# Kernel optimization log

Measured on AMD Instinct MI355X. Metric: run time of the kernel, lower is better.

The kernel has to match this reference:

```python
import jax, jax.numpy as jnp
import numpy as np
from jax import lax

GN_EPS = 1e-5


def _conv2d(x, w, b, pad):
    # x: (N, C, H, W), w: (O, I, kh, kw)
    y = lax.conv_general_dilated(x, w, window_strides=(1, 1),
                                 padding=[(pad, pad), (pad, pad)],
                                 dimension_numbers=('NCHW', 'OIHW', 'NCHW'))
    return y + b[None, :, None, None]


def _eca(x, eca_w, eca_b):
    # x: (N, C, H, W) -> channel attention (N, C, 1, 1)
    y = jnp.mean(x, axis=(2, 3))[:, None, :]  # (N, 1, C) : GAP then treat C as length
    y = lax.conv_general_dilated(y, eca_w, window_strides=(1,),
                                 padding=[(1, 1)],
                                 dimension_numbers=('NCH', 'OIH', 'NCH'))
    y = jax.nn.sigmoid(y + eca_b[None, :, None])  # (N, 1, C)
    return y[:, 0, :, None, None]  # (N, C, 1, 1)


def _group_norm_per_channel(x, gn_w, gn_b):
    # num_groups == num_channels: normalize each channel over (H, W)
    mean = jnp.mean(x, axis=(2, 3), keepdims=True)
    var = jnp.var(x, axis=(2, 3), keepdims=True)
    xhat = (x - mean) * lax.rsqrt(var + GN_EPS)
    return xhat * gn_w[None, :, None, None] + gn_b[None, :, None, None]


def setup_inputs() -> dict:
    key = jax.random.key(0)
    ks = jax.random.split(key, 8)
    b, c, h, w = 16, 512, 64, 64
    cg = c // 32  # 16
    s = 1.0 / np.sqrt(cg)
    return {
        'x': jax.random.normal(ks[0], (b, c, h, w), jnp.float32),
        'conv1x1_w': jax.random.normal(ks[1], (cg, cg, 1, 1), jnp.float32) * s,
        'conv1x1_b': jnp.zeros((cg,), jnp.float32),
        'conv3x3_w': jax.random.normal(ks[2], (cg, cg, 3, 3), jnp.float32) * (s / 3),
        'conv3x3_b': jnp.zeros((cg,), jnp.float32),
        'conv5x5_w': jax.random.normal(ks[3], (cg, cg, 5, 5), jnp.float32) * (s / 5),
        'conv5x5_b': jnp.zeros((cg,), jnp.float32),
        'gn_w': jnp.ones((cg,), jnp.float32),
        'gn_b': jnp.zeros((cg,), jnp.float32),
        'eca_w': jax.random.normal(ks[4], (1, 1, 3), jnp.float32) * 0.5,
        'eca_b': jnp.zeros((1,), jnp.float32),
        'groups': 32,
    }


def reference(x, conv1x1_w, conv1x1_b, conv3x3_w, conv3x3_b,
              conv5x5_w, conv5x5_b, gn_w, gn_b, eca_w, eca_b, groups):
    b, c, h, w = x.shape
    cg = c // groups
    bg = b * groups
    group_x = x.reshape(bg, cg, h, w)

    # coordinate attention branch
    x_h = jnp.mean(group_x, axis=3, keepdims=True)            # (bg, cg, h, 1)
    x_w = jnp.mean(group_x, axis=2, keepdims=True)            # (bg, cg, 1, w)
    x_w_t = jnp.transpose(x_w, (0, 1, 3, 2))                  # (bg, cg, w, 1)
    hw = _conv2d(jnp.concatenate([x_h, x_w_t], axis=2), conv1x1_w, conv1x1_b, 0)
    x_h2, x_w2 = hw[:, :, :h, :], hw[:, :, h:, :]             # (bg,cg,h,1), (bg,cg,w,1)
    gated = group_x * jax.nn.sigmoid(x_h2) * jax.nn.sigmoid(jnp.transpose(x_w2, (0, 1, 3, 2)))
    x1 = _group_norm_per_channel(gated, gn_w, gn_b)

    # parallel conv branches
    x2 = _conv2d(group_x, conv3x3_w, conv3x3_b, 1)
    x3 = _conv2d(group_x, conv5x5_w, conv5x5_b, 2)

    # shared ECA channel attention over the three branches
    ca = _eca(x1, eca_w, eca_b) + _eca(x2, eca_w, eca_b) + _eca(x3, eca_w, eca_b)
    group_x = group_x * ca

    # cross-scale softmax-bmm interactions
    def chan_softmax(v):
        # (bg, cg, h, w) -> softmax over channel means -> (bg, 1, cg)
        return jax.nn.softmax(jnp.mean(v, axis=(2, 3)), axis=-1)[:, None, :]

    x11, x21, x31 = chan_softmax(x1), chan_softmax(x2), chan_softmax(x3)
    f1 = x1.reshape(bg, cg, h * w)
    f2 = x2.reshape(bg, cg, h * w)
    f3 = x3.reshape(bg, cg, h * w)

    weights = (jnp.matmul(x11, f2) + jnp.matmul(x11, f3)
               + jnp.matmul(x21, f1) + jnp.matmul(x21, f3)
               + jnp.matmul(x31, f1) + jnp.matmul(x31, f2))  # (bg, 1, h*w)
    weights = jax.nn.sigmoid(weights.reshape(bg, 1, h, w))

    return (group_x * weights).reshape(b, c, h, w)
```

## Files before the change

kernel.cpp:

```cpp
#include <hip/hip_runtime.h>

typedef unsigned int u32;

#define CG  16
#define HWN 4096

__device__ __forceinline__ float sigm(float x) { return 1.0f / (1.0f + __expf(-x)); }

union SharedU {
  struct { float row[16][64]; float col[16][64]; float cpart[16][8][64]; } p0;
  struct { float row[16][64]; float col[16][64]; float RS[16][25]; float part2[16][16]; float part3[16][16]; } p1;
  float band[8][20][72];
};

__global__ __launch_bounds__(256, 2) void ema_kernel(
    const float* __restrict__ x,
    const float* __restrict__ w1, const float* __restrict__ b1,
    const float* __restrict__ w3, const float* __restrict__ b3,
    const float* __restrict__ w5, const float* __restrict__ b5,
    const float* __restrict__ gnw, const float* __restrict__ gnb,
    const float* __restrict__ ew, const float* __restrict__ eb,
    float* __restrict__ out)
{
  __shared__ SharedU U;
  __shared__ float s_sh[16][64];
  __shared__ float s_sw[16][64];
  __shared__ float s_W5[16][28];
  __shared__ float s_ca[16], s_A1[16], s_Cc[16];
  __shared__ float s_w1[256], s_b1[16], s_gnw[16], s_gnb[16], s_b3[16], s_b5[16], s_ecaw[3], s_ecab[1];
  __shared__ float s_m2[16], s_m3[16], s_sm1[16], s_sm2[16], s_sm3[16];
  __shared__ float s_a1[16], s_a2[16], s_a3[16], s_total[16];
  __shared__ float s_red[16][4][2];
  __shared__ float s_scal[2];

  const int g = blockIdx.x;
  const int t = threadIdx.x;
  const float* px   = x   + (size_t)g * CG * HWN;
  float*       pout = out + (size_t)g * CG * HWN;

  {
    const int j = t & 31, half = t >> 5;
    for (int c = 0; c < CG; ++c) {
      float ca0 = 0.f, ca1 = 0.f;
      for (int k = 0; k < 8; ++k) {
        const int y = half * 8 + k;
        float2 v = *(const float2*)(px + c * HWN + y * 64 + 2 * j);
        ca0 += v.x; ca1 += v.y;
        float rp = v.x + v.y;
        rp += __shfl_xor(rp, 1);  rp += __shfl_xor(rp, 2);
        rp += __shfl_xor(rp, 4);  rp += __shfl_xor(rp, 8);
        rp += __shfl_xor(rp, 16);
        if (j == 0) U.p0.row[c][y] = rp;
      }
      U.p0.cpart[c][half][2*j]   = ca0;
      U.p0.cpart[c][half][2*j+1] = ca1;
    }
  }
  s_w1[t] = w1[t];
  if (t < 16) {
    s_b1[t]  = b1[t];  s_gnw[t] = gnw[t]; s_gnb[t] = gnb[t];
    s_b3[t]  = b3[t];  s_b5[t]  = b5[t];
  }
  if (t < 3)  s_ecaw[t] = ew[t];
  if (t == 0) s_ecab[0] = eb[0];
  __syncthreads();

  for (int m = 0; m < 4; ++m) {
    int o = t + 256*m; int c = o >> 6, xx = o & 63;
    float s = 0.f;
    #pragma unroll
    for (int h = 0; h < 8; ++h) s += U.p0.cpart[c][h][xx];
    U.p0.col[c][xx] = s;
  }
  __syncthreads();
  if (t < 16) { float s = 0.f; for (int y = 0; y < 64; ++y) s += U.p1.row[t][y]; s_total[t] = s; }
  __syncthreads();

  for (int m = 0; m < 8; ++m) {
    int idx = t + 256*m; int o = idx >> 7, pos = idx & 127;
    float acc = s_b1[o];
    const float inv64 = 1.0f/64.0f;
    #pragma unroll
    for (int i = 0; i < 16; ++i) {
      float v = (pos < 64 ? U.p1.row[i][pos] : U.p1.col[i][pos-64]) * inv64;
      acc += s_w1[o*16+i] * v;
    }
    float sg = sigm(acc);
    if (pos < 64) s_sh[o][pos] = sg; else s_sw[o][pos-64] = sg;
  }
  for (int m = 0; m < 2; ++m) {
    int task = t + 256*m;
    if (task < 400) {
      int i = task / 25, kk = task % 25;
      int dy = kk/5 - 2, dx = kk%5 - 2;
      int a  = dy > 0 ? dy : 0,   b  = 64 + (dy < 0 ? dy : 0);
      int cl = dx > 0 ? dx : 0,   d  = 64 + (dx < 0 ? dx : 0);
      float S = s_total[i];
      if (a > 0)  S -= U.p1.row[i][0];
      if (a > 1)  S -= U.p1.row[i][1];
      if (b < 64) S -= U.p1.row[i][63];
      if (b < 63) S -= U.p1.row[i][62];
      for (int x0 = 0; x0 < cl; ++x0) {
        float cv = U.p1.col[i][x0];
        if (a > 0)  cv -= px[i*HWN + 0*64  + x0];
        if (a > 1)  cv -= px[i*HWN + 1*64  + x0];
        if (b < 64) cv -= px[i*HWN + 63*64 + x0];
        if (b < 63) cv -= px[i*HWN + 62*64 + x0];
        S -= cv;
      }
      for (int x0 = d; x0 < 64; ++x0) {
        float cv = U.p1.col[i][x0];
        if (a > 0)  cv -= px[i*HWN + 0*64  + x0];
        if (a > 1)  cv -= px[i*HWN + 1*64  + x0];
        if (b < 64) cv -= px[i*HWN + 63*64 + x0];
        if (b < 63) cv -= px[i*HWN + 62*64 + x0];
        S -= cv;
      }
      U.p1.RS[i][kk] = S;
    }
  }
  __syncthreads();

  {
    int o = t >> 4, i = t & 15;
    float p2 = 0.f, p3 = 0.f;
    const float* w3b = w3 + (o*16+i)*9;
    const float* w5b = w5 + (o*16+i)*25;
    #pragma unroll
    for (int ky = 0; ky < 3; ++ky)
      #pragma unroll
      for (int kx = 0; kx < 3; ++kx)
        p2 += w3b[ky*3+kx] * U.p1.RS[i][(ky+1)*5 + (kx+1)];
    #pragma unroll
    for (int kk = 0; kk < 25; ++kk) p3 += w5b[kk] * U.p1.RS[i][kk];
    U.p1.part2[o][i] = p2; U.p1.part3[o][i] = p3;
  }
  __syncthreads();
  if (t < 16)      { float s=0.f; for (int i=0;i<16;++i) s += U.p1.part2[t][i];    s_m2[t] = s_b3[t] + s*(1.0f/4096.0f); }
  else if (t < 32) { int o=t-16; float s=0.f; for (int i=0;i<16;++i) s += U.p1.part3[o][i]; s_m3[o] = s_b5[o] + s*(1.0f/4096.0f); }
  __syncthreads();

  if (t < 3) {
    const float* m = (t==0) ? s_gnb : (t==1) ? s_m2 : s_m3;
    float* dst     = (t==0) ? s_sm1 : (t==1) ? s_sm2 : s_sm3;
    float mx = m[0];
    for (int c = 1; c < 16; ++c) mx = fmaxf(mx, m[c]);
    float e[16], ssum = 0.f;
    for (int c = 0; c < 16; ++c) { e[c] = __expf(m[c]-mx); ssum += e[c]; }
    float r = 1.0f/ssum;
    for (int c = 0; c < 16; ++c) dst[c] = e[c]*r;
  }
  __syncthreads();

  if (t < 16) {
    int c = t;
    float casum = 0.f;
    #pragma unroll
    for (int v = 0; v < 3; ++v) {
      const float* m = (v==0) ? s_gnb : (v==1) ? s_m2 : s_m3;
      float acc = s_ecab[0] + s_ecaw[1]*m[c];
      if (c > 0)  acc += s_ecaw[0]*m[c-1];
      if (c < 15) acc += s_ecaw[2]*m[c+1];
      casum += sigm(acc);
    }
    s_ca[c] = casum;
    s_a1[c] = s_sm2[c] + s_sm3[c];
    s_a2[c] = s_sm1[c] + s_sm3[c];
    s_a3[c] = s_sm1[c] + s_sm2[c];
  }
  __syncthreads();

  if (t == 0) {
    float s = 0.f;
    for (int o = 0; o < 16; ++o) s += s_a2[o]*s_b3[o] + s_a3[o]*s_b5[o];
    s_scal[1] = s;
  }
  for (int m = 0; m < 2; ++m) {
    int task = t + 256*m;
    if (task < 400) {
      int i = task/25, kk = task%25, ky = kk/5, kx = kk%5;
      float acc = 0.f;
      #pragma unroll
      for (int o = 0; o < 16; ++o) acc += s_a3[o]*w5[((o*16+i)*5+ky)*5+kx];
      if (ky >= 1 && ky <= 3 && kx >= 1 && kx <= 3) {
        #pragma unroll
        for (int o = 0; o < 16; ++o) acc += s_a2[o]*w3[((o*16+i)*3+(ky-1))*3+(kx-1)];
      }
      s_W5[i][kk] = acc;
    }
  }
  __syncthreads();

  {
    const int x0 = (t & 7) * 8;
    const int yA = t >> 3, yB = yA + 32;
    const int wv4 = t >> 6;
    #pragma unroll 1
    for (int c = 0; c < 16; ++c) {
      float sw8[8];
      #pragma unroll
      for (int i = 0; i < 8; ++i) sw8[i] = s_sw[c][x0+i];
      float shA = s_sh[c][yA], shB = s_sh[c][yB];
      float4 a0 = *(const float4*)(px + c*HWN + yA*64 + x0);
      float4 a1 = *(const float4*)(px + c*HWN + yA*64 + x0 + 4);
      float4 b0 = *(const float4*)(px + c*HWN + yB*64 + x0);
      float4 b1 = *(const float4*)(px + c*HWN + yB*64 + x0 + 4);
      float va[8] = {a0.x,a0.y,a0.z,a0.w,a1.x,a1.y,a1.z,a1.w};
      float vb[8] = {b0.x,b0.y,b0.z,b0.w,b1.x,b1.y,b1.z,b1.w};
      float gsl = 0.f, gql = 0.f;
      #pragma unroll
      for (int i = 0; i < 8; ++i) {
        float ga = va[i] * shA * sw8[i];
        float gb = vb[i] * shB * sw8[i];
        gsl += ga + gb; gql += ga*ga + gb*gb;
      }
      float a = gsl, b2 = gql;
      a += __shfl_xor(a, 1);  b2 += __shfl_xor(b2, 1);
      a += __shfl_xor(a, 2);  b2 += __shfl_xor(b2, 2);
      a += __shfl_xor(a, 4);  b2 += __shfl_xor(b2, 4);
      a += __shfl_xor(a, 8);  b2 += __shfl_xor(b2, 8);
      a += __shfl_xor(a, 16); b2 += __shfl_xor(b2, 16);
      a += __shfl_xor(a, 32); b2 += __shfl_xor(b2, 32);
      if ((t & 63) == 0) { s_red[c][wv4][0] = a; s_red[c][wv4][1] = b2; }
    }
  }
  __syncthreads();
  if (t < 16) {
    int c = t;
    float S = 0.f, Q = 0.f;
    #pragma unroll
    for (int w = 0; w < 4; ++w) { S += s_red[c][w][0]; Q += s_red[c][w][1]; }
    float mu  = S * (1.0f/4096.0f);
    float var = Q * (1.0f/4096.0f) - mu*mu;
    float inv = rsqrtf(var + 1e-5f);
    s_A1[c] = s_a1[c] * s_gnw[c] * inv;
    s_Cc[c] = s_a1[c] * (s_gnb[c] - mu * s_gnw[c] * inv);
  }
  __syncthreads();
  if (t == 0) { float s = s_scal[1]; for (int c = 0; c < 16; ++c) s += s_Cc[c]; s_scal[0] = s; }
  for (int m = 0; m < 4; ++m) { int idx = t + 256*m; int c = idx >> 6, y = idx & 63; s_sh[c][y] *= s_A1[c]; }
  __syncthreads();

  for (int m = 0; m < 12; ++m) { int idx = t + 256*m; if (idx < 2880) ((float4*)U.band)[idx] = make_float4(0.f,0.f,0.f,0.f); }
  __syncthreads();

  const int lane = t & 63, wv = t >> 6;
  const float Cc = s_scal[0];
  for (int band = 0; band < 4; ++band) {
    const int yb = band * 16;
    float ws[4] = {Cc, Cc, Cc, Cc};
    for (int half = 0; half < 2; ++half) {
      __syncthreads();
      for (int k = 0; k < 10; ++k) {
        int q = t + 256*k;
        int rr = q >> 4, xc = (q & 15) * 4;
        int c = rr / 20, yy = rr % 20;
        int y = yb + yy - 2;
        float4 v = make_float4(0.f,0.f,0.f,0.f);
        if ((unsigned)y < 64u) v = *(const float4*)(px + (half*8+c)*HWN + y*64 + xc);
        *(float4*)&U.band[c][yy][4 + xc] = v;
      }
      __syncthreads();

      #pragma unroll 1
      for (int c = 0; c < 8; ++c) {
        const int ch = half*8 + c;
        float Wk[25];
        #pragma unroll
        for (int kk = 0; kk < 25; ++kk) Wk[kk] = s_W5[ch][kk];
        float swv = s_sw[ch][lane];
        float ash[4];
        #pragma unroll
        for (int r = 0; r < 4; ++r) ash[r] = s_sh[ch][yb + 4*wv + r];
        const float* bp = &U.band[c][4*wv][lane + 2];
        #pragma unroll
        for (int q = 0; q < 8; ++q) {
          const float* rowp = bp + q*72;
          float v0 = rowp[0];
          float v1 = rowp[1];
          float v2 = rowp[2];
          float v3 = rowp[3];
          float v4 = rowp[4];
          #pragma unroll
          for (int r = 0; r < 4; ++r) {
            const int kr = q - r;
            if (kr >= 0 && kr <= 4) {
              ws[r] += Wk[kr*5+0]*v0 + Wk[kr*5+1]*v1 + Wk[kr*5+2]*v2 + Wk[kr*5+3]*v3 + Wk[kr*5+4]*v4;
              if (kr == 2) ws[r] += ash[r] * (v2 * swv);
            }
          }
        }
      }
    }
    #pragma unroll
    for (int r = 0; r < 4; ++r) {
      float sg = sigm(ws[r]);
      int y = yb + 4*wv + r;
      const float* xp = px   + y*64 + lane;
      float*       op = pout + y*64 + lane;
      #pragma unroll
      for (int c = 0; c < 16; ++c) {
        op[c*HWN] = xp[c*HWN] * s_ca[c] * sg;
      }
    }
  }
}

extern "C" void kernel_launch(void* const* d_in, const int* in_sizes, int n_in,
                              void* d_out, int out_size, void* d_ws, size_t ws_size,
                              hipStream_t stream) {
  const float* X  = (const float*)d_in[0];
  const float* W1 = (const float*)d_in[1];
  const float* B1 = (const float*)d_in[2];
  const float* W3 = (const float*)d_in[3];
  const float* B3 = (const float*)d_in[4];
  const float* W5 = (const float*)d_in[5];
  const float* B5 = (const float*)d_in[6];
  const float* GW = (const float*)d_in[7];
  const float* GB = (const float*)d_in[8];
  const float* EW = (const float*)d_in[9];
  const float* EB = (const float*)d_in[10];
  float* O = (float*)d_out;
  ema_kernel<<<dim3(512), dim3(256), 0, stream>>>(X, W1, B1, W3, B3, W5, B5, GW, GB, EW, EB, O);
}
```

Before: 402.8 us.

## Fuse GN stats into double-buffered 5x5 conv pass with 4x4 register tiles

Restructures the main stencil phase so each thread computes a 4x4 output tile across all 16 channels, with whole-channel planes staged into a double-buffered padded LDS array while the previous channel is computed. The group-norm statistics are gathered in the same pass instead of a separate read of x. The gated term then needs its own extra pass over x once the GN scale is known. The initial row/column reductions switch to float4 loads with shuffle-based column sums. This trades more registers (ws/gws arrays) and an extra per-channel barrier for fewer global reloads and better register-level data reuse in the stencil.

```diff
diff --git a/kernel.cpp b/kernel.cpp
--- a/kernel.cpp
+++ b/kernel.cpp
@@ -2,15 +2,22 @@
 
 typedef unsigned int u32;
 
-#define CG  16
-#define HWN 4096
+#define CG   16
+#define HWN  4096
+#define LSTR 72
 
 __device__ __forceinline__ float sigm(float x) { return 1.0f / (1.0f + __expf(-x)); }
 
 union SharedU {
-  struct { float row[16][64]; float col[16][64]; float cpart[16][8][64]; } p0;
-  struct { float row[16][64]; float col[16][64]; float RS[16][25]; float part2[16][16]; float part3[16][16]; } p1;
-  float band[8][20][72];
+  struct {
+    float row[16][64];
+    float col[16][64];
+    union {
+      float cwave[16][4][64];
+      struct { float RS[16][25]; float part2[16][16]; float part3[16][16]; } r;
+    } u;
+  } p;
+  float cb[2][68][LSTR];
 };
 
 __global__ __launch_bounds__(256, 2) void ema_kernel(
@@ -39,21 +46,24 @@
   float*       pout = out + (size_t)g * CG * HWN;
 
   {
-    const int j = t & 31, half = t >> 5;
+    const int j4 = t & 15, hh = t >> 4, wv4 = t >> 6;
     for (int c = 0; c < CG; ++c) {
-      float ca0 = 0.f, ca1 = 0.f;
-      for (int k = 0; k < 8; ++k) {
-        const int y = half * 8 + k;
-        float2 v = *(const float2*)(px + c * HWN + y * 64 + 2 * j);
-        ca0 += v.x; ca1 += v.y;
-        float rp = v.x + v.y;
-        rp += __shfl_xor(rp, 1);  rp += __shfl_xor(rp, 2);
-        rp += __shfl_xor(rp, 4);  rp += __shfl_xor(rp, 8);
-        rp += __shfl_xor(rp, 16);
-        if (j == 0) U.p0.row[c][y] = rp;
-      }
-      U.p0.cpart[c][half][2*j]   = ca0;
-      U.p0.cpart[c][half][2*j+1] = ca1;
+      float cp0 = 0.f, cp1 = 0.f, cp2 = 0.f, cp3 = 0.f;
+      #pragma unroll
+      for (int k = 0; k < 4; ++k) {
+        int y = 4 * hh + k;
+        float4 v = *(const float4*)(px + c * HWN + y * 64 + 4 * j4);
+        float rs = v.x + v.y + v.z + v.w;
+        rs += __shfl_xor(rs, 1); rs += __shfl_xor(rs, 2);
+        rs += __shfl_xor(rs, 4); rs += __shfl_xor(rs, 8);
+        if (j4 == 0) U.p.row[c][y] = rs;
+        cp0 += v.x; cp1 += v.y; cp2 += v.z; cp3 += v.w;
+      }
+      cp0 += __shfl_xor(cp0, 16); cp0 += __shfl_xor(cp0, 32);
+      cp1 += __shfl_xor(cp1, 16); cp1 += __shfl_xor(cp1, 32);
+      cp2 += __shfl_xor(cp2, 16); cp2 += __shfl_xor(cp2, 32);
+      cp3 += __shfl_xor(cp3, 16); cp3 += __shfl_xor(cp3, 32);
+      if ((t & 48) == 0) *(float4*)&U.p.u.cwave[c][wv4][4 * j4] = make_float4(cp0, cp1, cp2, cp3);
     }
   }
   s_w1[t] = w1[t];
@@ -65,58 +75,61 @@
   if (t == 0) s_ecab[0] = eb[0];
   __syncthreads();
 
-  for (int m = 0; m < 4; ++m) {
-    int o = t + 256*m; int c = o >> 6, xx = o & 63;
-    float s = 0.f;
-    #pragma unroll
-    for (int h = 0; h < 8; ++h) s += U.p0.cpart[c][h][xx];
-    U.p0.col[c][xx] = s;
-  }
-  __syncthreads();
-  if (t < 16) { float s = 0.f; for (int y = 0; y < 64; ++y) s += U.p1.row[t][y]; s_total[t] = s; }
+  {
+    int c = t >> 4, q = t & 15;
+    float4 s = make_float4(0.f, 0.f, 0.f, 0.f);
+    #pragma unroll
+    for (int w = 0; w < 4; ++w) {
+      float4 v = *(float4*)&U.p.u.cwave[c][w][4 * q];
+      s.x += v.x; s.y += v.y; s.z += v.z; s.w += v.w;
+    }
+    *(float4*)&U.p.col[c][4 * q] = s;
+  }
+  __syncthreads();
+  if (t < 16) { float s = 0.f; for (int y = 0; y < 64; ++y) s += U.p.row[t][y]; s_total[t] = s; }
   __syncthreads();
 
   for (int m = 0; m < 8; ++m) {
-    int idx = t + 256*m; int o = idx >> 7, pos = idx & 127;
+    int idx = t + 256 * m; int o = idx >> 7, pos = idx & 127;
     float acc = s_b1[o];
-    const float inv64 = 1.0f/64.0f;
+    const float inv64 = 1.0f / 64.0f;
     #pragma unroll
     for (int i = 0; i < 16; ++i) {
-      float v = (pos < 64 ? U.p1.row[i][pos] : U.p1.col[i][pos-64]) * inv64;
-      acc += s_w1[o*16+i] * v;
+      float v = (pos < 64 ? U.p.row[i][pos] : U.p.col[i][pos - 64]) * inv64;
+      acc += s_w1[o * 16 + i] * v;
     }
     float sg = sigm(acc);
-    if (pos < 64) s_sh[o][pos] = sg; else s_sw[o][pos-64] = sg;
+    if (pos < 64) s_sh[o][pos] = sg; else s_sw[o][pos - 64] = sg;
   }
   for (int m = 0; m < 2; ++m) {
-    int task = t + 256*m;
+    int task = t + 256 * m;
     if (task < 400) {
       int i = task / 25, kk = task % 25;
-      int dy = kk/5 - 2, dx = kk%5 - 2;
+      int dy = kk / 5 - 2, dx = kk % 5 - 2;
       int a  = dy > 0 ? dy : 0,   b  = 64 + (dy < 0 ? dy : 0);
       int cl = dx > 0 ? dx : 0,   d  = 64 + (dx < 0 ? dx : 0);
       float S = s_total[i];
-      if (a > 0)  S -= U.p1.row[i][0];
-      if (a > 1)  S -= U.p1.row[i][1];
-      if (b < 64) S -= U.p1.row[i][63];
-      if (b < 63) S -= U.p1.row[i][62];
+      if (a > 0)  S -= U.p.row[i][0];
+      if (a > 1)  S -= U.p.row[i][1];
+      if (b < 64) S -= U.p.row[i][63];
+      if (b < 63) S -= U.p.row[i][62];
       for (int x0 = 0; x0 < cl; ++x0) {
-        float cv = U.p1.col[i][x0];
-        if (a > 0)  cv -= px[i*HWN + 0*64  + x0];
-        if (a > 1)  cv -= px[i*HWN + 1*64  + x0];
-        if (b < 64) cv -= px[i*HWN + 63*64 + x0];
-        if (b < 63) cv -= px[i*HWN + 62*64 + x0];
+        float cv = U.p.col[i][x0];
+        if (a > 0)  cv -= px[i * HWN + 0 * 64  + x0];
+        if (a > 1)  cv -= px[i * HWN + 1 * 64  + x0];
+        if (b < 64) cv -= px[i * HWN + 63 * 64 + x0];
+        if (b < 63) cv -= px[i * HWN + 62 * 64 + x0];
         S -= cv;
       }
       for (int x0 = d; x0 < 64; ++x0) {
-        float cv = U.p1.col[i][x0];
-        if (a > 0)  cv -= px[i*HWN + 0*64  + x0];
-        if (a > 1)  cv -= px[i*HWN + 1*64  + x0];
-        if (b < 64) cv -= px[i*HWN + 63*64 + x0];
-        if (b < 63) cv -= px[i*HWN + 62*64 + x0];
+        float cv = U.p.col[i][x0];
+        if (a > 0)  cv -= px[i * HWN + 0 * 64  + x0];
+        if (a > 1)  cv -= px[i * HWN + 1 * 64  + x0];
+        if (b < 64) cv -= px[i * HWN + 63 * 64 + x0];
+        if (b < 63) cv -= px[i * HWN + 62 * 64 + x0];
         S -= cv;
       }
-      U.p1.RS[i][kk] = S;
+      U.p.u.r.RS[i][kk] = S;
     }
   }
   __syncthreads();
@@ -124,31 +137,31 @@
   {
     int o = t >> 4, i = t & 15;
     float p2 = 0.f, p3 = 0.f;
-    const float* w3b = w3 + (o*16+i)*9;
-    const float* w5b = w5 + (o*16+i)*25;
+    const float* w3b = w3 + (o * 16 + i) * 9;
+    const float* w5b = w5 + (o * 16 + i) * 25;
     #pragma unroll
     for (int ky = 0; ky < 3; ++ky)
       #pragma unroll
       for (int kx = 0; kx < 3; ++kx)
-        p2 += w3b[ky*3+kx] * U.p1.RS[i][(ky+1)*5 + (kx+1)];
-    #pragma unroll
-    for (int kk = 0; kk < 25; ++kk) p3 += w5b[kk] * U.p1.RS[i][kk];
-    U.p1.part2[o][i] = p2; U.p1.part3[o][i] = p3;
-  }
-  __syncthreads();
-  if (t < 16)      { float s=0.f; for (int i=0;i<16;++i) s += U.p1.part2[t][i];    s_m2[t] = s_b3[t] + s*(1.0f/4096.0f); }
-  else if (t < 32) { int o=t-16; float s=0.f; for (int i=0;i<16;++i) s += U.p1.part3[o][i]; s_m3[o] = s_b5[o] + s*(1.0f/4096.0f); }
+        p2 += w3b[ky * 3 + kx] * U.p.u.r.RS[i][(ky + 1) * 5 + (kx + 1)];
+    #pragma unroll
+    for (int kk = 0; kk < 25; ++kk) p3 += w5b[kk] * U.p.u.r.RS[i][kk];
+    U.p.u.r.part2[o][i] = p2; U.p.u.r.part3[o][i] = p3;
+  }
+  __syncthreads();
+  if (t < 16)      { float s = 0.f; for (int i = 0; i < 16; ++i) s += U.p.u.r.part2[t][i];    s_m2[t] = s_b3[t] + s * (1.0f/4096.0f); }
+  else if (t < 32) { int o = t - 16; float s = 0.f; for (int i = 0; i < 16; ++i) s += U.p.u.r.part3[o][i]; s_m3[o] = s_b5[o] + s * (1.0f/4096.0f); }
   __syncthreads();
 
   if (t < 3) {
-    const float* m = (t==0) ? s_gnb : (t==1) ? s_m2 : s_m3;
-    float* dst     = (t==0) ? s_sm1 : (t==1) ? s_sm2 : s_sm3;
+    const float* m = (t == 0) ? s_gnb : (t == 1) ? s_m2 : s_m3;
+    float* dst     = (t == 0) ? s_sm1 : (t == 1) ? s_sm2 : s_sm3;
     float mx = m[0];
     for (int c = 1; c < 16; ++c) mx = fmaxf(mx, m[c]);
     float e[16], ssum = 0.f;
-    for (int c = 0; c < 16; ++c) { e[c] = __expf(m[c]-mx); ssum += e[c]; }
-    float r = 1.0f/ssum;
-    for (int c = 0; c < 16; ++c) dst[c] = e[c]*r;
+    for (int c = 0; c < 16; ++c) { e[c] = __expf(m[c] - mx); ssum += e[c]; }
+    float r = 1.0f / ssum;
+    for (int c = 0; c < 16; ++c) dst[c] = e[c] * r;
   }
   __syncthreads();
 
@@ -157,10 +170,10 @@
     float casum = 0.f;
     #pragma unroll
     for (int v = 0; v < 3; ++v) {
-      const float* m = (v==0) ? s_gnb : (v==1) ? s_m2 : s_m3;
-      float acc = s_ecab[0] + s_ecaw[1]*m[c];
-      if (c > 0)  acc += s_ecaw[0]*m[c-1];
-      if (c < 15) acc += s_ecaw[2]*m[c+1];
+      const float* m = (v == 0) ? s_gnb : (v == 1) ? s_m2 : s_m3;
+      float acc = s_ecab[0] + s_ecaw[1] * m[c];
+      if (c > 0)  acc += s_ecaw[0] * m[c - 1];
+      if (c < 15) acc += s_ecaw[2] * m[c + 1];
       casum += sigm(acc);
     }
     s_ca[c] = casum;
@@ -172,136 +185,147 @@
 
   if (t == 0) {
     float s = 0.f;
-    for (int o = 0; o < 16; ++o) s += s_a2[o]*s_b3[o] + s_a3[o]*s_b5[o];
+    for (int o = 0; o < 16; ++o) s += s_a2[o] * s_b3[o] + s_a3[o] * s_b5[o];
     s_scal[1] = s;
   }
   for (int m = 0; m < 2; ++m) {
-    int task = t + 256*m;
+    int task = t + 256 * m;
     if (task < 400) {
-      int i = task/25, kk = task%25, ky = kk/5, kx = kk%5;
+      int i = task / 25, kk = task % 25, ky = kk / 5, kx = kk % 5;
       float acc = 0.f;
       #pragma unroll
-      for (int o = 0; o < 16; ++o) acc += s_a3[o]*w5[((o*16+i)*5+ky)*5+kx];
+      for (int o = 0; o < 16; ++o) acc += s_a3[o] * w5[((o * 16 + i) * 5 + ky) * 5 + kx];
       if (ky >= 1 && ky <= 3 && kx >= 1 && kx <= 3) {
         #pragma unroll
-        for (int o = 0; o < 16; ++o) acc += s_a2[o]*w3[((o*16+i)*3+(ky-1))*3+(kx-1)];
+        for (int o = 0; o < 16; ++o) acc += s_a2[o] * w3[((o * 16 + i) * 3 + (ky - 1)) * 3 + (kx - 1)];
       }
       s_W5[i][kk] = acc;
     }
-  }
-  __syncthreads();
-
-  {
-    const int x0 = (t & 7) * 8;
-    const int yA = t >> 3, yB = yA + 32;
-    const int wv4 = t >> 6;
-    #pragma unroll 1
-    for (int c = 0; c < 16; ++c) {
-      float sw8[8];
+    else if (task < 448) { int i = (task - 400) / 3; s_W5[i][25 + (task - 400) % 3] = 0.f; }
+  }
+  __syncthreads();
+
+  for (int m = 0; m < 10; ++m) { int idx = t + 256 * m; if (idx < 2448) ((float4*)U.cb)[idx] = make_float4(0.f, 0.f, 0.f, 0.f); }
+  __syncthreads();
+
+  const int x0 = 4 * (t & 15), y0 = 4 * (t >> 4), wv4 = t >> 6;
+
+  #define STAGE(buf, c) {                                              \
+    _Pragma("unroll")                                                  \
+    for (int k = 0; k < 4; ++k) {                                      \
+      int q = t + 256 * k;                                             \
+      int rr = q >> 4, xc = (q & 15) * 4;                              \
+      float4 v = *(const float4*)(px + (c) * HWN + rr * 64 + xc);      \
+      float* d = &U.cb[buf][2 + rr][2 + xc];                           \
+      *(float2*)d       = make_float2(v.x, v.y);                       \
+      *(float2*)(d + 2) = make_float2(v.z, v.w);                       \
+    }                                                                  \
+  }
+
+  float ws[16];
+  #pragma unroll
+  for (int i = 0; i < 16; ++i) ws[i] = 0.f;
+
+  STAGE(0, 0);
+  __syncthreads();
+  #pragma unroll 1
+  for (int c = 0; c < 16; ++c) {
+    if (c < 15) STAGE((c + 1) & 1, c + 1);
+    float Wk[28];
+    #pragma unroll
+    for (int i = 0; i < 7; ++i) *(float4*)&Wk[4 * i] = *(float4*)&s_W5[c][4 * i];
+    float shv[4], swv[4];
+    #pragma unroll
+    for (int r = 0; r < 4; ++r) { shv[r] = s_sh[c][y0 + r]; swv[r] = s_sw[c][x0 + r]; }
+    const float* base = &U.cb[c & 1][0][0];
+    float gsl = 0.f, gql = 0.f;
+    #pragma unroll
+    for (int q = 0; q < 8; ++q) {
+      const float* rp = base + (y0 + q) * LSTR + x0;
+      float4 A = *(const float4*)rp, B = *(const float4*)(rp + 4);
+      float v[8] = {A.x, A.y, A.z, A.w, B.x, B.y, B.z, B.w};
+      if (q >= 2 && q <= 5) {
+        const int ry = q - 2;
+        #pragma unroll
+        for (int m = 0; m < 4; ++m) { float gg = v[m + 2] * shv[ry] * swv[m]; gsl += gg; gql += gg * gg; }
+      }
       #pragma unroll
-      for (int i = 0; i < 8; ++i) sw8[i] = s_sw[c][x0+i];
-      float shA = s_sh[c][yA], shB = s_sh[c][yB];
-      float4 a0 = *(const float4*)(px + c*HWN + yA*64 + x0);
-      float4 a1 = *(const float4*)(px + c*HWN + yA*64 + x0 + 4);
-      float4 b0 = *(const float4*)(px + c*HWN + yB*64 + x0);
-      float4 b1 = *(const float4*)(px + c*HWN + yB*64 + x0 + 4);
-      float va[8] = {a0.x,a0.y,a0.z,a0.w,a1.x,a1.y,a1.z,a1.w};
-      float vb[8] = {b0.x,b0.y,b0.z,b0.w,b1.x,b1.y,b1.z,b1.w};
-      float gsl = 0.f, gql = 0.f;
-      #pragma unroll
-      for (int i = 0; i < 8; ++i) {
-        float ga = va[i] * shA * sw8[i];
-        float gb = vb[i] * shB * sw8[i];
-        gsl += ga + gb; gql += ga*ga + gb*gb;
-      }
-      float a = gsl, b2 = gql;
-      a += __shfl_xor(a, 1);  b2 += __shfl_xor(b2, 1);
-      a += __shfl_xor(a, 2);  b2 += __shfl_xor(b2, 2);
-      a += __shfl_xor(a, 4);  b2 += __shfl_xor(b2, 4);
-      a += __shfl_xor(a, 8);  b2 += __shfl_xor(b2, 8);
-      a += __shfl_xor(a, 16); b2 += __shfl_xor(b2, 16);
-      a += __shfl_xor(a, 32); b2 += __shfl_xor(b2, 32);
-      if ((t & 63) == 0) { s_red[c][wv4][0] = a; s_red[c][wv4][1] = b2; }
-    }
-  }
-  __syncthreads();
+      for (int r = 0; r < 4; ++r) {
+        if (q - r >= 0 && q - r <= 4) {
+          const int kr = q - r;
+          #pragma unroll
+          for (int m = 0; m < 4; ++m) {
+            float a = ws[4 * r + m];
+            a += Wk[kr * 5 + 0] * v[m + 0];
+            a += Wk[kr * 5 + 1] * v[m + 1];
+            a += Wk[kr * 5 + 2] * v[m + 2];
+            a += Wk[kr * 5 + 3] * v[m + 3];
+            a += Wk[kr * 5 + 4] * v[m + 4];
+            ws[4 * r + m] = a;
+          }
+        }
+      }
+    }
+    gsl += __shfl_xor(gsl, 1);  gql += __shfl_xor(gql, 1);
+    gsl += __shfl_xor(gsl, 2);  gql += __shfl_xor(gql, 2);
+    gsl += __shfl_xor(gsl, 4);  gql += __shfl_xor(gql, 4);
+    gsl += __shfl_xor(gsl, 8);  gql += __shfl_xor(gql, 8);
+    gsl += __shfl_xor(gsl, 16); gql += __shfl_xor(gql, 16);
+    gsl += __shfl_xor(gsl, 32); gql += __shfl_xor(gql, 32);
+    if ((t & 63) == 0) { s_red[c][wv4][0] = gsl; s_red[c][wv4][1] = gql; }
+    __syncthreads();
+  }
+
   if (t < 16) {
     int c = t;
     float S = 0.f, Q = 0.f;
     #pragma unroll
     for (int w = 0; w < 4; ++w) { S += s_red[c][w][0]; Q += s_red[c][w][1]; }
-    float mu  = S * (1.0f/4096.0f);
-    float var = Q * (1.0f/4096.0f) - mu*mu;
+    float mu  = S * (1.0f / 4096.0f);
+    float var = Q * (1.0f / 4096.0f) - mu * mu;
     float inv = rsqrtf(var + 1e-5f);
     s_A1[c] = s_a1[c] * s_gnw[c] * inv;
     s_Cc[c] = s_a1[c] * (s_gnb[c] - mu * s_gnw[c] * inv);
   }
   __syncthreads();
   if (t == 0) { float s = s_scal[1]; for (int c = 0; c < 16; ++c) s += s_Cc[c]; s_scal[0] = s; }
-  for (int m = 0; m < 4; ++m) { int idx = t + 256*m; int c = idx >> 6, y = idx & 63; s_sh[c][y] *= s_A1[c]; }
-  __syncthreads();
-
-  for (int m = 0; m < 12; ++m) { int idx = t + 256*m; if (idx < 2880) ((float4*)U.band)[idx] = make_float4(0.f,0.f,0.f,0.f); }
-  __syncthreads();
-
-  const int lane = t & 63, wv = t >> 6;
-  const float Cc = s_scal[0];
-  for (int band = 0; band < 4; ++band) {
-    const int yb = band * 16;
-    float ws[4] = {Cc, Cc, Cc, Cc};
-    for (int half = 0; half < 2; ++half) {
-      __syncthreads();
-      for (int k = 0; k < 10; ++k) {
-        int q = t + 256*k;
-        int rr = q >> 4, xc = (q & 15) * 4;
-        int c = rr / 20, yy = rr % 20;
-        int y = yb + yy - 2;
-        float4 v = make_float4(0.f,0.f,0.f,0.f);
-        if ((unsigned)y < 64u) v = *(const float4*)(px + (half*8+c)*HWN + y*64 + xc);
-        *(float4*)&U.band[c][yy][4 + xc] = v;
-      }
-      __syncthreads();
-
-      #pragma unroll 1
-      for (int c = 0; c < 8; ++c) {
-        const int ch = half*8 + c;
-        float Wk[25];
-        #pragma unroll
-        for (int kk = 0; kk < 25; ++kk) Wk[kk] = s_W5[ch][kk];
-        float swv = s_sw[ch][lane];
-        float ash[4];
-        #pragma unroll
-        for (int r = 0; r < 4; ++r) ash[r] = s_sh[ch][yb + 4*wv + r];
-        const float* bp = &U.band[c][4*wv][lane + 2];
-        #pragma unroll
-        for (int q = 0; q < 8; ++q) {
-          const float* rowp = bp + q*72;
-          float v0 = rowp[0];
-          float v1 = rowp[1];
-          float v2 = rowp[2];
-          float v3 = rowp[3];
-          float v4 = rowp[4];
-          #pragma unroll
-          for (int r = 0; r < 4; ++r) {
-            const int kr = q - r;
-            if (kr >= 0 && kr <= 4) {
-              ws[r] += Wk[kr*5+0]*v0 + Wk[kr*5+1]*v1 + Wk[kr*5+2]*v2 + Wk[kr*5+3]*v3 + Wk[kr*5+4]*v4;
-              if (kr == 2) ws[r] += ash[r] * (v2 * swv);
-            }
-          }
-        }
-      }
-    }
+  for (int m = 0; m < 4; ++m) { int idx = t + 256 * m; int c = idx >> 6, y = idx & 63; s_sh[c][y] *= s_A1[c]; }
+  __syncthreads();
+
+  float gws[16];
+  #pragma unroll
+  for (int i = 0; i < 16; ++i) gws[i] = 0.f;
+  #pragma unroll 1
+  for (int c = 0; c < 16; ++c) {
+    float shv[4], swv[4];
+    #pragma unroll
+    for (int r = 0; r < 4; ++r) { shv[r] = s_sh[c][y0 + r]; swv[r] = s_sw[c][x0 + r]; }
     #pragma unroll
     for (int r = 0; r < 4; ++r) {
-      float sg = sigm(ws[r]);
-      int y = yb + 4*wv + r;
-      const float* xp = px   + y*64 + lane;
-      float*       op = pout + y*64 + lane;
-      #pragma unroll
-      for (int c = 0; c < 16; ++c) {
-        op[c*HWN] = xp[c*HWN] * s_ca[c] * sg;
-      }
+      float4 xv = *(const float4*)(px + c * HWN + (y0 + r) * 64 + x0);
+      gws[4 * r + 0] += shv[r] * swv[0] * xv.x;
+      gws[4 * r + 1] += shv[r] * swv[1] * xv.y;
+      gws[4 * r + 2] += shv[r] * swv[2] * xv.z;
+      gws[4 * r + 3] += shv[r] * swv[3] * xv.w;
+    }
+  }
+  {
+    const float Cc = s_scal[0];
+    #pragma unroll
+    for (int i = 0; i < 16; ++i) ws[i] = sigm(ws[i] + gws[i] + Cc);
+  }
+  #pragma unroll 1
+  for (int c = 0; c < 16; ++c) {
+    float cav = s_ca[c];
+    #pragma unroll
+    for (int r = 0; r < 4; ++r) {
+      float4 xv = *(const float4*)(px + c * HWN + (y0 + r) * 64 + x0);
+      float4 o;
+      o.x = xv.x * cav * ws[4 * r + 0];
+      o.y = xv.y * cav * ws[4 * r + 1];
+      o.z = xv.z * cav * ws[4 * r + 2];
+      o.w = xv.w * cav * ws[4 * r + 3];
+      *(float4*)(pout + c * HWN + (y0 + r) * 64 + x0) = o;
     }
   }
 }
```

Measured after the change: 345.5 us. 14.2% less time.
